# Optimization experiments

Measured on AMD Instinct MI355X. Metric: run time of the kernel, lower is better.

## Reference

```python
import jax, jax.numpy as jnp
import numpy as np

D_MODEL = 1024
NUM_HEADS = 16
HEAD_DIM = D_MODEL // NUM_HEADS


def setup_inputs() -> dict:
    key = jax.random.key(0)
    k_x, k_qw, k_qb, k_ow, k_ob = jax.random.split(key, 5)
    s = 1.0 / np.sqrt(D_MODEL)
    return {
        "x": jax.random.normal(k_x, (2, 2048, D_MODEL), dtype=jnp.float32),
        "qkv_w": jax.random.uniform(k_qw, (3 * D_MODEL, D_MODEL), jnp.float32, -s, s),
        "qkv_b": jax.random.uniform(k_qb, (3 * D_MODEL,), jnp.float32, -s, s),
        "out_w": jax.random.uniform(k_ow, (D_MODEL, D_MODEL), jnp.float32, -s, s),
        "out_b": jax.random.uniform(k_ob, (D_MODEL,), jnp.float32, -s, s),
    }


def reference(x, qkv_w, qkv_b, out_w, out_b):
    B, S, D = x.shape
    # fused QKV projection: [B,S,3D]
    qkv = jnp.einsum("bsd,ed->bse", x, qkv_w) + qkv_b
    # [B,S,H,3*hd] -> [B,H,S,3*hd]
    qkv = qkv.reshape(B, S, NUM_HEADS, 3 * HEAD_DIM).transpose(0, 2, 1, 3)
    q, k, v = jnp.split(qkv, 3, axis=-1)
    scale = 1.0 / jnp.sqrt(jnp.asarray(HEAD_DIM, x.dtype))
    scores = jnp.einsum("bhqd,bhkd->bhqk", q, k) * scale
    attn = jax.nn.softmax(scores, axis=-1)
    vals = jnp.einsum("bhqk,bhkd->bhqd", attn, v)
    vals = vals.transpose(0, 2, 1, 3).reshape(B, S, D)
    return jnp.einsum("bsd,ed->bse", vals, out_w) + out_b
```

## Files before the change

### kernel.cpp

```cpp
#include <hip/hip_runtime.h>
#include <stdint.h>


#define D_MODEL 1024
#define NUM_HEADS 16
#define HEAD_DIM 64
#define BATCH 2
#define SEQ 2048
#define M_TOT (BATCH * SEQ)
#define QKV_N (3 * D_MODEL)

typedef __attribute__((ext_vector_type(8))) short bf16x8;
typedef __attribute__((ext_vector_type(4))) short bf16x4;
typedef __attribute__((ext_vector_type(4))) float f32x4;
typedef __attribute__((ext_vector_type(4))) unsigned int u32x4;

__device__ __forceinline__ unsigned short f2bf(float f) {
    union { float f; unsigned int u; } v; v.f = f;
    unsigned int u = v.u;
    u += 0x7fffu + ((u >> 16) & 1u);
    return (unsigned short)(u >> 16);
}

__device__ __forceinline__ unsigned int exp2_bf16u(float x) {
    return (unsigned int)__builtin_fmaf(x, 128.0f, 16251.58f);
}

__device__ __forceinline__ unsigned int perm_pack(unsigned int hi, unsigned int lo) {
#if __has_builtin(__builtin_amdgcn_perm)
    return __builtin_amdgcn_perm(hi, lo, 0x05040100u);
#else
    return (lo & 0xFFFFu) | (hi << 16);
#endif
}

__device__ __forceinline__ void gld_lds16(const unsigned short* g,
                                          unsigned short* l) {
#if __has_builtin(__builtin_amdgcn_global_load_lds)
    __builtin_amdgcn_global_load_lds(
        (const __attribute__((address_space(1))) unsigned int*)g,
        (__attribute__((address_space(3))) unsigned int*)l, 16, 0, 0);
#else
    *(u32x4*)(l + (threadIdx.x & 63) * 8) = *(const u32x4*)g;
#endif
}

__global__ __launch_bounds__(256) void cvt_all(const float* __restrict__ x,
                                               const float* __restrict__ qw,
                                               const float* __restrict__ ow,
                                               unsigned short* __restrict__ xb,
                                               unsigned short* __restrict__ wqb,
                                               unsigned short* __restrict__ wob) {
    int i = blockIdx.x * 256 + threadIdx.x;
    const int N1 = M_TOT * D_MODEL / 8;
    const int N2 = N1 + QKV_N * D_MODEL / 8;
    const float* src; unsigned short* dst; int j;
    if (i < N1)      { src = x;  dst = xb;  j = i; }
    else if (i < N2) { src = qw; dst = wqb; j = i - N1; }
    else             { src = ow; dst = wob; j = i - N2; }
    const float4* s = (const float4*)src;
    float4 a = s[2 * j], b = s[2 * j + 1];
    u32x4 o;
    o.x = (unsigned int)f2bf(a.x) | ((unsigned int)f2bf(a.y) << 16);
    o.y = (unsigned int)f2bf(a.z) | ((unsigned int)f2bf(a.w) << 16);
    o.z = (unsigned int)f2bf(b.x) | ((unsigned int)f2bf(b.y) << 16);
    o.w = (unsigned int)f2bf(b.z) | ((unsigned int)f2bf(b.w) << 16);
    *(u32x4*)(dst + 8 * (size_t)j) = o;
}

__device__ __forceinline__ void gemm_tile(const unsigned short* __restrict__ A,
                                          const unsigned short* __restrict__ Bw,
                                          int K, int m0, int n0,
                                          unsigned short (*As)[128 * 64],
                                          unsigned short (*Bs)[128 * 64],
                                          f32x4 acc[4][4]) {
    const int tid = threadIdx.x;
    const int lane = tid & 63;
    const int wave = tid >> 6;
    const int wm = (wave >> 1) * 64;
    const int wn = (wave & 1) * 64;
    const int quad = lane >> 4;
    const int l16 = lane & 15;
    const int lrow = lane >> 3;
    const int sw = (lane & 7) ^ (lrow & 7);
    const int l7 = l16 & 7;

#pragma unroll
    for (int mt = 0; mt < 4; mt++)
#pragma unroll
        for (int nt = 0; nt < 4; nt++) acc[mt][nt] = (f32x4)0.0f;

    auto stage = [&](int kt, int b) {
#pragma unroll
        for (int i = 0; i < 4; ++i) {
            int R = wave * 32 + i * 8;
            int grow = R + lrow;
            gld_lds16(A + (size_t)(m0 + grow) * K + kt + sw * 8, As[b] + R * 64);
            gld_lds16(Bw + (size_t)(n0 + grow) * K + kt + sw * 8, Bs[b] + R * 64);
        }
    };

    stage(0, 0);
    __syncthreads();

    const int NT = K / 64;
    for (int t = 0; t < NT; ++t) {
        const int cur = t & 1;
        if (t + 1 < NT) stage((t + 1) * 64, cur ^ 1);
#pragma unroll
        for (int ks = 0; ks < 2; ++ks) {
            int cxl = ((ks * 4 + quad) ^ l7) * 8;
            bf16x8 af[4], bf[4];
#pragma unroll
            for (int mt = 0; mt < 4; mt++)
                af[mt] = *(const bf16x8*)(As[cur] + (wm + mt * 16 + l16) * 64 + cxl);
#pragma unroll
            for (int nt = 0; nt < 4; nt++)
                bf[nt] = *(const bf16x8*)(Bs[cur] + (wn + nt * 16 + l16) * 64 + cxl);
#pragma unroll
            for (int mt = 0; mt < 4; mt++)
#pragma unroll
                for (int nt = 0; nt < 4; nt++)
                    acc[mt][nt] = __builtin_amdgcn_mfma_f32_16x16x32_bf16(
                        af[mt], bf[nt], acc[mt][nt], 0, 0, 0);
        }
        __syncthreads();
    }
}

__global__ __launch_bounds__(256) void gemm_qkv(const unsigned short* __restrict__ xb,
                                                const unsigned short* __restrict__ wb,
                                                const float* __restrict__ bias,
                                                unsigned short* __restrict__ qb,
                                                unsigned short* __restrict__ kb,
                                                unsigned short* __restrict__ vtb) {
    __shared__ __align__(16) unsigned short As[2][128 * 64];
    __shared__ __align__(16) unsigned short Bs[2][128 * 64];
    f32x4 acc[4][4];
    const int m0 = blockIdx.y * 128, n0 = blockIdx.x * 128;
    gemm_tile(xb, wb, D_MODEL, m0, n0, As, Bs, acc);

    const int tid = threadIdx.x;
    const int lane = tid & 63, wave = tid >> 6;
    const int wm = (wave >> 1) * 64, wn = (wave & 1) * 64;
    const int quad = lane >> 4, l16 = lane & 15;
    const float QSCALE = 0.18033688011112042f;

    const int s64 = (n0 + wn) >> 6;
    const int h = s64 / 3;
    const int sec = s64 - h * 3;
    const int bh = (m0 >> 11) * NUM_HEADS + h;
    const int sbase = (m0 + wm) & 2047;

    unsigned short* sm = ((wave & 2) ? Bs[0] : As[0]) + (wave & 1) * 4096;

    if (sec < 2) {
        const float scl = (sec == 0) ? QSCALE : 1.0f;
#pragma unroll
        for (int nt = 0; nt < 4; nt++) {
            int c = nt * 16 + l16;
            float bia = bias[n0 + wn + c];
#pragma unroll
            for (int mt = 0; mt < 4; mt++)
#pragma unroll
                for (int r = 0; r < 4; r++) {
                    int row = mt * 16 + quad * 4 + r;
                    sm[row * 64 + ((((c >> 3) ^ (row & 7)) << 3) | (c & 7))] =
                        f2bf((acc[mt][nt][r] + bia) * scl);
                }
        }
        unsigned short* dstb = (sec == 0) ? qb : kb;
#pragma unroll
        for (int p = 0; p < 8; p++) {
            int row = p * 8 + (lane >> 3);
            int g = lane & 7;
            u32x4 ch = *(const u32x4*)(sm + row * 64 + ((g ^ (row & 7)) << 3));
            *(u32x4*)(dstb + ((size_t)bh * SEQ + sbase + row) * 64 + g * 8) = ch;
        }
    } else {
#pragma unroll
        for (int nt = 0; nt < 4; nt++) {
            int d = nt * 16 + l16;
            float bia = bias[n0 + wn + d];
#pragma unroll
            for (int mt = 0; mt < 4; mt++) {
                int c = mt * 16 + quad * 4;
                unsigned short t4[4];
#pragma unroll
                for (int r = 0; r < 4; r++) t4[r] = f2bf(acc[mt][nt][r] + bia);
                *(uint64_t*)(sm + d * 64 +
                             ((((c >> 3) ^ (d & 7)) << 3) | (c & 7))) =
                    *(const uint64_t*)t4;
            }
        }
#pragma unroll
        for (int p = 0; p < 8; p++) {
            int row = p * 8 + (lane >> 3);
            int g = lane & 7;
            u32x4 ch = *(const u32x4*)(sm + row * 64 + ((g ^ (row & 7)) << 3));
            *(u32x4*)(vtb + ((size_t)bh * 64 + row) * SEQ + sbase + g * 8) = ch;
        }
    }
}

__global__ __launch_bounds__(256) void attn(const unsigned short* __restrict__ qb,
                                            const unsigned short* __restrict__ kb,
                                            const unsigned short* __restrict__ vtb,
                                            unsigned short* __restrict__ vals) {
    __shared__ __align__(16) unsigned short Ks[2][2][64 * 64];
    __shared__ __align__(16) unsigned short VTs[2][2][64 * 64];

    const int tid = threadIdx.x;
    const int lane = tid & 63, wave = tid >> 6;
    const int quad = lane >> 4, l16 = lane & 15;
    const int l7 = l16 & 7;
    const int bh = blockIdx.x;
    const int q0 = blockIdx.y * 128;
    const unsigned short* qh = qb + (size_t)bh * SEQ * 64;
    const unsigned short* kh = kb + (size_t)bh * SEQ * 64;
    const unsigned short* vth = vtb + (size_t)bh * 64 * SEQ;
    const int wrow = wave * 32;

    bf16x8 aq[2][2];
#pragma unroll
    for (int nq = 0; nq < 2; nq++)
#pragma unroll
        for (int ks = 0; ks < 2; ++ks)
            aq[nq][ks] = *(const bf16x8*)(
                qh + (size_t)(q0 + wrow + nq * 16 + l16) * 64 + ks * 32 + quad * 8);

    const int lrow = lane >> 3;
    const int sw = (lane & 7) ^ (lrow & 7);

    int cxl0 = ((0 * 4 + quad) ^ l7) * 8;
    int cxl1 = ((1 * 4 + quad) ^ l7) * 8;

    auto stage = [&](int t, int b) {
        int kt = t * 128;
#pragma unroll
        for (int h = 0; h < 2; ++h) {
            int kth = kt + h * 64;
#pragma unroll
            for (int i = 0; i < 2; ++i) {
                int R = wave * 16 + i * 8;
                int row = R + lrow;
                int krow = (row & 0x23) | ((row & 0x0C) << 1) | ((row & 0x10) >> 2);
                gld_lds16(kh + (size_t)(kth + krow) * 64 + sw * 8,
                          &Ks[b][h][R * 64]);
                gld_lds16(vth + (size_t)row * SEQ + kth + sw * 8,
                          &VTs[b][h][R * 64]);
            }
        }
    };

    stage(0, 0);
    __syncthreads();

    f32x4 oacc[2][4];
    f32x4 lsum[2];
#pragma unroll
    for (int mt = 0; mt < 2; mt++) {
        lsum[mt] = (f32x4)0.0f;
#pragma unroll
        for (int nt = 0; nt < 4; nt++) oacc[mt][nt] = (f32x4)0.0f;
    }

    bf16x8 ones8;
#pragma unroll
    for (int j = 0; j < 8; j++) ones8[j] = (short)0x3F80;

    const int NR = SEQ / 128;
    for (int t = 0; t < NR; ++t) {
        const int cur = t & 1;
        if (t + 1 < NR) stage(t + 1, cur ^ 1);

#pragma unroll
        for (int hf = 0; hf < 2; ++hf) {
            const unsigned short* Kc = Ks[cur][hf];
            const unsigned short* Vc = VTs[cur][hf];

            f32x4 sacc[4][2];
#pragma unroll
            for (int mk = 0; mk < 4; mk++)
#pragma unroll
                for (int nq = 0; nq < 2; nq++) sacc[mk][nq] = (f32x4)0.0f;
#pragma unroll
            for (int ks = 0; ks < 2; ++ks) {
                int cxl = ks ? cxl1 : cxl0;
                bf16x8 bk[4];
#pragma unroll
                for (int mk = 0; mk < 4; mk++)
                    bk[mk] = *(const bf16x8*)(Kc + (mk * 16 + l16) * 64 + cxl);
#pragma unroll
                for (int mk = 0; mk < 4; mk++)
#pragma unroll
                    for (int nq = 0; nq < 2; nq++)
                        sacc[mk][nq] = __builtin_amdgcn_mfma_f32_16x16x32_bf16(
                            bk[mk], aq[nq][ks], sacc[mk][nq], 0, 0, 0);
            }

            bf16x4 pf[4][2];
#pragma unroll
            for (int mk = 0; mk < 4; mk++)
#pragma unroll
                for (int nq = 0; nq < 2; nq++) {
                    unsigned int u0 = exp2_bf16u(sacc[mk][nq][0]);
                    unsigned int u1 = exp2_bf16u(sacc[mk][nq][1]);
                    unsigned int u2 = exp2_bf16u(sacc[mk][nq][2]);
                    unsigned int u3 = exp2_bf16u(sacc[mk][nq][3]);
                    union { unsigned int u[2]; bf16x4 b; } cv;
                    cv.u[0] = perm_pack(u1, u0);
                    cv.u[1] = perm_pack(u3, u2);
                    pf[mk][nq] = cv.b;
                }

#pragma unroll
            for (int w = 0; w < 2; ++w) {
                bf16x8 ap0 = __builtin_shufflevector(
                    pf[2 * w][0], pf[2 * w + 1][0], 0, 1, 2, 3, 4, 5, 6, 7);
                bf16x8 ap1 = __builtin_shufflevector(
                    pf[2 * w][1], pf[2 * w + 1][1], 0, 1, 2, 3, 4, 5, 6, 7);
                int cxl = w ? cxl1 : cxl0;
#pragma unroll
                for (int nt = 0; nt < 4; nt++) {
                    bf16x8 bv = *(const bf16x8*)(Vc + (nt * 16 + l16) * 64 + cxl);
                    oacc[0][nt] = __builtin_amdgcn_mfma_f32_16x16x32_bf16(
                        ap0, bv, oacc[0][nt], 0, 0, 0);
                    oacc[1][nt] = __builtin_amdgcn_mfma_f32_16x16x32_bf16(
                        ap1, bv, oacc[1][nt], 0, 0, 0);
                }
                lsum[0] = __builtin_amdgcn_mfma_f32_16x16x32_bf16(
                    ap0, ones8, lsum[0], 0, 0, 0);
                lsum[1] = __builtin_amdgcn_mfma_f32_16x16x32_bf16(
                    ap1, ones8, lsum[1], 0, 0, 0);
            }
        }
        __syncthreads();
    }

    const int b = bh >> 4, h = bh & 15;
#pragma unroll
    for (int mt = 0; mt < 2; mt++) {
        f32x4 inv;
#pragma unroll
        for (int r = 0; r < 4; r++) inv[r] = 1.0f / lsum[mt][r];
#pragma unroll
        for (int nt = 0; nt < 4; nt++) {
            int d = nt * 16 + l16;
#pragma unroll
            for (int r = 0; r < 4; r++) {
                int row = wrow + mt * 16 + quad * 4 + r;
                float v = oacc[mt][nt][r] * inv[r];
                vals[((size_t)(b * SEQ + q0 + row)) * D_MODEL + h * 64 + d] =
                    f2bf(v);
            }
        }
    }
}

__global__ __launch_bounds__(256) void gemm_out(const unsigned short* __restrict__ vb,
                                                const unsigned short* __restrict__ wb,
                                                const float* __restrict__ bias,
                                                float* __restrict__ out) {
    __shared__ __align__(16) unsigned short As[2][128 * 64];
    __shared__ __align__(16) unsigned short Bs[2][64 * 64];
    const int tid = threadIdx.x;
    const int lane = tid & 63, wave = tid >> 6;
    const int wm = (wave >> 1) * 64, wn = (wave & 1) * 32;
    const int quad = lane >> 4, l16 = lane & 15;
    const int lrow = lane >> 3;
    const int sw = (lane & 7) ^ (lrow & 7);
    const int l7 = l16 & 7;
    const int m0 = blockIdx.y * 128, n0 = blockIdx.x * 64;

    f32x4 acc[4][2];
#pragma unroll
    for (int mt = 0; mt < 4; mt++)
#pragma unroll
        for (int nt = 0; nt < 2; nt++) acc[mt][nt] = (f32x4)0.0f;

    auto stage = [&](int kt, int b) {
#pragma unroll
        for (int i = 0; i < 4; ++i) {
            int R = wave * 32 + i * 8;
            gld_lds16(vb + (size_t)(m0 + R + lrow) * D_MODEL + kt + sw * 8,
                      As[b] + R * 64);
        }
#pragma unroll
        for (int i = 0; i < 2; ++i) {
            int R = wave * 16 + i * 8;
            gld_lds16(wb + (size_t)(n0 + R + lrow) * D_MODEL + kt + sw * 8,
                      Bs[b] + R * 64);
        }
    };

    stage(0, 0);
    __syncthreads();

    const int NT = D_MODEL / 64;
    for (int t = 0; t < NT; ++t) {
        const int cur = t & 1;
        if (t + 1 < NT) stage((t + 1) * 64, cur ^ 1);
#pragma unroll
        for (int ks = 0; ks < 2; ++ks) {
            int cxl = ((ks * 4 + quad) ^ l7) * 8;
            bf16x8 af[4], bf[2];
#pragma unroll
            for (int mt = 0; mt < 4; mt++)
                af[mt] = *(const bf16x8*)(As[cur] + (wm + mt * 16 + l16) * 64 + cxl);
#pragma unroll
            for (int nt = 0; nt < 2; nt++)
                bf[nt] = *(const bf16x8*)(Bs[cur] + (wn + nt * 16 + l16) * 64 + cxl);
#pragma unroll
            for (int mt = 0; mt < 4; mt++)
#pragma unroll
                for (int nt = 0; nt < 2; nt++)
                    acc[mt][nt] = __builtin_amdgcn_mfma_f32_16x16x32_bf16(
                        af[mt], bf[nt], acc[mt][nt], 0, 0, 0);
        }
        __syncthreads();
    }

#pragma unroll
    for (int mt = 0; mt < 4; mt++)
#pragma unroll
        for (int nt = 0; nt < 2; nt++) {
            int n = n0 + wn + nt * 16 + l16;
            float bia = bias[n];
#pragma unroll
            for (int r = 0; r < 4; r++) {
                int m = m0 + wm + mt * 16 + quad * 4 + r;
                out[(size_t)m * D_MODEL + n] = acc[mt][nt][r] + bia;
            }
        }
}

extern "C" void kernel_launch(void* const* d_in, const int* in_sizes, int n_in,
                              void* d_out, int out_size, void* d_ws, size_t ws_size,
                              hipStream_t stream) {
    const float* x = (const float*)d_in[0];
    const float* qkv_w = (const float*)d_in[1];
    const float* qkv_b = (const float*)d_in[2];
    const float* out_w = (const float*)d_in[3];
    const float* out_b = (const float*)d_in[4];
    float* out = (float*)d_out;

    char* ws = (char*)d_ws;
    size_t off = 0;
    auto carve = [&](size_t bytes) -> void* {
        void* p = ws + off;
        off += (bytes + 255) & ~(size_t)255;
        return p;
    };
    unsigned short* xb  = (unsigned short*)carve((size_t)M_TOT * D_MODEL * 2);
    unsigned short* wqb = (unsigned short*)carve((size_t)QKV_N * D_MODEL * 2);
    unsigned short* wob = (unsigned short*)carve((size_t)D_MODEL * D_MODEL * 2);
    unsigned short* qbuf = (unsigned short*)carve((size_t)M_TOT * D_MODEL * 2);
    unsigned short* kbuf = (unsigned short*)carve((size_t)M_TOT * D_MODEL * 2);
    unsigned short* vtb  = (unsigned short*)carve((size_t)M_TOT * D_MODEL * 2);
    unsigned short* vals = xb;

    const int NCHUNK = (M_TOT + QKV_N + D_MODEL) * D_MODEL / 8;
    cvt_all<<<NCHUNK / 256, 256, 0, stream>>>(x, qkv_w, out_w, xb, wqb, wob);

    gemm_qkv<<<dim3(QKV_N / 128, M_TOT / 128), 256, 0, stream>>>(
        xb, wqb, qkv_b, qbuf, kbuf, vtb);

    attn<<<dim3(BATCH * NUM_HEADS, SEQ / 128), 256, 0, stream>>>(
        qbuf, kbuf, vtb, vals);

    gemm_out<<<dim3(D_MODEL / 64, M_TOT / 128), 256, 0, stream>>>(
        vals, wob, out_b, out);
}
```

Baseline: 184.6 us.

## Retile QKV GEMM to 256x192 per-head blocks with finer-grained pipelined loads

The QKV projection GEMM now uses 512-thread blocks computing 256x192 tiles, so each block covers one full head (Q, K and V slices). This replaces the 128x128 tiles with 256 threads. The K loop splits staging into quarter-steps with explicit vmcnt waits and raw barriers, and raises wave priority around the MFMA bursts so loads overlap compute. The epilogue writes Q, K and transposed V for the whole head through shared memory in one pass. The aim is better operand reuse and less barrier stall, at the cost of more registers per thread, larger LDS use, and reliance on hand-counted waitcnt values.

Result: faster. 171.4 us (-7.2%).

```diff
diff --git a/kernel.cpp b/kernel.cpp
--- a/kernel.cpp
+++ b/kernel.cpp
@@ -68,138 +68,150 @@
     *(u32x4*)(dst + 8 * (size_t)j) = o;
 }
 
-__device__ __forceinline__ void gemm_tile(const unsigned short* __restrict__ A,
-                                          const unsigned short* __restrict__ Bw,
-                                          int K, int m0, int n0,
-                                          unsigned short (*As)[128 * 64],
-                                          unsigned short (*Bs)[128 * 64],
-                                          f32x4 acc[4][4]) {
-    const int tid = threadIdx.x;
-    const int lane = tid & 63;
-    const int wave = tid >> 6;
-    const int wm = (wave >> 1) * 64;
-    const int wn = (wave & 1) * 64;
-    const int quad = lane >> 4;
-    const int l16 = lane & 15;
-    const int lrow = lane >> 3;
-    const int sw = (lane & 7) ^ (lrow & 7);
-    const int l7 = l16 & 7;
-
-#pragma unroll
-    for (int mt = 0; mt < 4; mt++)
-#pragma unroll
-        for (int nt = 0; nt < 4; nt++) acc[mt][nt] = (f32x4)0.0f;
-
-    auto stage = [&](int kt, int b) {
-#pragma unroll
-        for (int i = 0; i < 4; ++i) {
-            int R = wave * 32 + i * 8;
-            int grow = R + lrow;
-            gld_lds16(A + (size_t)(m0 + grow) * K + kt + sw * 8, As[b] + R * 64);
-            gld_lds16(Bw + (size_t)(n0 + grow) * K + kt + sw * 8, Bs[b] + R * 64);
-        }
-    };
-
-    stage(0, 0);
-    __syncthreads();
-
-    const int NT = K / 64;
-    for (int t = 0; t < NT; ++t) {
-        const int cur = t & 1;
-        if (t + 1 < NT) stage((t + 1) * 64, cur ^ 1);
-#pragma unroll
-        for (int ks = 0; ks < 2; ++ks) {
-            int cxl = ((ks * 4 + quad) ^ l7) * 8;
-            bf16x8 af[4], bf[4];
-#pragma unroll
-            for (int mt = 0; mt < 4; mt++)
-                af[mt] = *(const bf16x8*)(As[cur] + (wm + mt * 16 + l16) * 64 + cxl);
-#pragma unroll
-            for (int nt = 0; nt < 4; nt++)
-                bf[nt] = *(const bf16x8*)(Bs[cur] + (wn + nt * 16 + l16) * 64 + cxl);
-#pragma unroll
-            for (int mt = 0; mt < 4; mt++)
-#pragma unroll
-                for (int nt = 0; nt < 4; nt++)
-                    acc[mt][nt] = __builtin_amdgcn_mfma_f32_16x16x32_bf16(
-                        af[mt], bf[nt], acc[mt][nt], 0, 0, 0);
-        }
-        __syncthreads();
-    }
-}
-
-__global__ __launch_bounds__(256) void gemm_qkv(const unsigned short* __restrict__ xb,
-                                                const unsigned short* __restrict__ wb,
-                                                const float* __restrict__ bias,
-                                                unsigned short* __restrict__ qb,
-                                                unsigned short* __restrict__ kb,
-                                                unsigned short* __restrict__ vtb) {
-    __shared__ __align__(16) unsigned short As[2][128 * 64];
-    __shared__ __align__(16) unsigned short Bs[2][128 * 64];
-    f32x4 acc[4][4];
-    const int m0 = blockIdx.y * 128, n0 = blockIdx.x * 128;
-    gemm_tile(xb, wb, D_MODEL, m0, n0, As, Bs, acc);
+__global__ __launch_bounds__(512, 2) void gemm_qkv(const unsigned short* __restrict__ xb,
+                                                   const unsigned short* __restrict__ wb,
+                                                   const float* __restrict__ bias,
+                                                   unsigned short* __restrict__ qb,
+                                                   unsigned short* __restrict__ kb,
+                                                   unsigned short* __restrict__ vtb) {
+    __shared__ __align__(16) unsigned short L[57344];
 
     const int tid = threadIdx.x;
     const int lane = tid & 63, wave = tid >> 6;
-    const int wm = (wave >> 1) * 64, wn = (wave & 1) * 64;
-    const int quad = lane >> 4, l16 = lane & 15;
+    const int quad = lane >> 4, l16 = lane & 15, l7 = l16 & 7;
+    const int lrow = lane >> 3;
+    const int sw = (lane & 7) ^ lrow;
+    const int m0 = blockIdx.x * 256;
+    const int n0 = blockIdx.y * 192;
+    const int wmr = (wave >> 2) * 128;
+    const int wn = (wave & 3) * 48;
+
+    float biasr[3];
+#pragma unroll
+    for (int nt = 0; nt < 3; nt++) biasr[nt] = bias[n0 + wn + nt * 16 + l16];
+
+    f32x4 acc[8][3];
+#pragma unroll
+    for (int m = 0; m < 8; m++)
+#pragma unroll
+        for (int nt = 0; nt < 3; nt++) acc[m][nt] = (f32x4)0.0f;
+
+    auto stA = [&](int tt, int s, int b) {
+        int R = s * 64 + wave * 8 + lrow;
+        gld_lds16(xb + (size_t)(m0 + R) * D_MODEL + tt * 64 + sw * 8,
+                  L + b * 16384 + (s * 64 + wave * 8) * 64);
+    };
+    auto stB = [&](int tt, int s, int b) {
+        int R = s * 64 + wave * 8 + lrow;
+        gld_lds16(wb + (size_t)(n0 + R) * D_MODEL + tt * 64 + sw * 8,
+                  L + 32768 + b * 12288 + (s * 64 + wave * 8) * 64);
+    };
+
+    stB(0, 0, 0); stB(0, 1, 0); stB(0, 2, 0);
+    stA(0, 0, 0); stA(0, 1, 0); stA(0, 2, 0); stA(0, 3, 0);
+
+    const int NT = D_MODEL / 64;
+    for (int t = 0; t < NT; ++t) {
+        const int cb = t & 1, nb = cb ^ 1;
+        const int tn = (t + 1 < NT) ? t + 1 : NT - 1;
+        const unsigned short* Ac = L + cb * 16384;
+        const unsigned short* Bc = L + 32768 + cb * 12288;
+        bf16x8 bfr[3][2];
+
+#pragma unroll
+        for (int q = 0; q < 4; ++q) {
+            if (q == 0) {
+                asm volatile("s_waitcnt vmcnt(1)" ::: "memory");
+                asm volatile("s_barrier" ::: "memory");
+            } else if (q == 2) {
+                asm volatile("s_waitcnt vmcnt(4)" ::: "memory");
+                asm volatile("s_barrier" ::: "memory");
+            }
+            if (q == 0)      { stB(tn, 0, nb); stB(tn, 1, nb); }
+            else if (q == 1) { stB(tn, 2, nb); stA(tn, 0, nb); }
+            else if (q == 2) { stA(tn, 1, nb); stA(tn, 2, nb); }
+            else             { stA(tn, 3, nb); }
+
+            if (q == 0) {
+#pragma unroll
+                for (int nt = 0; nt < 3; nt++)
+#pragma unroll
+                    for (int ks = 0; ks < 2; ++ks)
+                        bfr[nt][ks] = *(const bf16x8*)(
+                            Bc + (wn + nt * 16 + l16) * 64 + ((ks * 4 + quad) ^ l7) * 8);
+            }
+            bf16x8 afr[2][2];
+#pragma unroll
+            for (int j = 0; j < 2; ++j)
+#pragma unroll
+                for (int ks = 0; ks < 2; ++ks)
+                    afr[j][ks] = *(const bf16x8*)(
+                        Ac + (wmr + (q * 2 + j) * 16 + l16) * 64 + ((ks * 4 + quad) ^ l7) * 8);
+
+            __builtin_amdgcn_s_setprio(1);
+#pragma unroll
+            for (int j = 0; j < 2; ++j)
+#pragma unroll
+                for (int nt = 0; nt < 3; nt++)
+#pragma unroll
+                    for (int ks = 0; ks < 2; ++ks)
+                        acc[q * 2 + j][nt] = __builtin_amdgcn_mfma_f32_16x16x32_bf16(
+                            afr[j][ks], bfr[nt][ks], acc[q * 2 + j][nt], 0, 0, 0);
+            __builtin_amdgcn_s_setprio(0);
+        }
+    }
+
+    __syncthreads();
+
     const float QSCALE = 0.18033688011112042f;
-
-    const int s64 = (n0 + wn) >> 6;
-    const int h = s64 / 3;
-    const int sec = s64 - h * 3;
-    const int bh = (m0 >> 11) * NUM_HEADS + h;
-    const int sbase = (m0 + wm) & 2047;
-
-    unsigned short* sm = ((wave & 2) ? Bs[0] : As[0]) + (wave & 1) * 4096;
-
-    if (sec < 2) {
-        const float scl = (sec == 0) ? QSCALE : 1.0f;
-#pragma unroll
-        for (int nt = 0; nt < 4; nt++) {
-            int c = nt * 16 + l16;
-            float bia = bias[n0 + wn + c];
-#pragma unroll
-            for (int mt = 0; mt < 4; mt++)
+#pragma unroll
+    for (int nt = 0; nt < 3; nt++) {
+        int colb = wn + nt * 16;
+        int sec = colb >> 6;
+        int c64 = (colb & 63) + l16;
+        float bia = biasr[nt];
+        if (sec < 2) {
+            unsigned short* img = L + sec * 16384;
+            float scl = sec ? 1.0f : QSCALE;
+#pragma unroll
+            for (int mt = 0; mt < 8; mt++)
 #pragma unroll
                 for (int r = 0; r < 4; r++) {
-                    int row = mt * 16 + quad * 4 + r;
-                    sm[row * 64 + ((((c >> 3) ^ (row & 7)) << 3) | (c & 7))] =
+                    int row = wmr + mt * 16 + quad * 4 + r;
+                    img[row * 64 + ((((c64 >> 3) ^ (row & 7)) << 3) | (c64 & 7))] =
                         f2bf((acc[mt][nt][r] + bia) * scl);
                 }
-        }
-        unsigned short* dstb = (sec == 0) ? qb : kb;
-#pragma unroll
-        for (int p = 0; p < 8; p++) {
-            int row = p * 8 + (lane >> 3);
-            int g = lane & 7;
-            u32x4 ch = *(const u32x4*)(sm + row * 64 + ((g ^ (row & 7)) << 3));
-            *(u32x4*)(dstb + ((size_t)bh * SEQ + sbase + row) * 64 + g * 8) = ch;
-        }
-    } else {
-#pragma unroll
-        for (int nt = 0; nt < 4; nt++) {
-            int d = nt * 16 + l16;
-            float bia = bias[n0 + wn + d];
-#pragma unroll
-            for (int mt = 0; mt < 4; mt++) {
-                int c = mt * 16 + quad * 4;
+        } else {
+            unsigned short* img = L + 32768;
+            int d = c64;
+#pragma unroll
+            for (int mt = 0; mt < 8; mt++) {
+                int cs = wmr + mt * 16 + quad * 4;
+                int sb = cs >> 6, c64s = cs & 63;
                 unsigned short t4[4];
 #pragma unroll
                 for (int r = 0; r < 4; r++) t4[r] = f2bf(acc[mt][nt][r] + bia);
-                *(uint64_t*)(sm + d * 64 +
-                             ((((c >> 3) ^ (d & 7)) << 3) | (c & 7))) =
+                *(uint64_t*)(img + (d * 4 + sb) * 64 +
+                             ((((c64s >> 3) ^ (d & 7)) << 3) | (c64s & 7))) =
                     *(const uint64_t*)t4;
             }
         }
-#pragma unroll
-        for (int p = 0; p < 8; p++) {
-            int row = p * 8 + (lane >> 3);
-            int g = lane & 7;
-            u32x4 ch = *(const u32x4*)(sm + row * 64 + ((g ^ (row & 7)) << 3));
-            *(u32x4*)(vtb + ((size_t)bh * 64 + row) * SEQ + sbase + g * 8) = ch;
-        }
+    }
+    __syncthreads();
+
+    const int bh = (m0 >> 11) * NUM_HEADS + blockIdx.y;
+    const int sbase = m0 & 2047;
+    const int g = lane & 7;
+#pragma unroll
+    for (int p = 0; p < 4; p++) {
+        int rr = p * 64 + wave * 8 + (lane >> 3);
+        u32x4 ch = *(const u32x4*)(L + rr * 64 + ((g ^ (rr & 7)) << 3));
+        *(u32x4*)(qb + ((size_t)bh * SEQ + sbase + rr) * 64 + g * 8) = ch;
+        ch = *(const u32x4*)(L + 16384 + rr * 64 + ((g ^ (rr & 7)) << 3));
+        *(u32x4*)(kb + ((size_t)bh * SEQ + sbase + rr) * 64 + g * 8) = ch;
+        int d = rr >> 2, sb = rr & 3;
+        ch = *(const u32x4*)(L + 32768 + rr * 64 + ((g ^ (d & 7)) << 3));
+        *(u32x4*)(vtb + ((size_t)bh * 64 + d) * SEQ + sbase + sb * 64 + g * 8) = ch;
     }
 }
 
@@ -463,7 +475,7 @@
     const int NCHUNK = (M_TOT + QKV_N + D_MODEL) * D_MODEL / 8;
     cvt_all<<<NCHUNK / 256, 256, 0, stream>>>(x, qkv_w, out_w, xb, wqb, wob);
 
-    gemm_qkv<<<dim3(QKV_N / 128, M_TOT / 128), 256, 0, stream>>>(
+    gemm_qkv<<<dim3(M_TOT / 256, QKV_N / 192), 512, 0, stream>>>(
         xb, wqb, qkv_b, qbuf, kbuf, vtb);
 
     attn<<<dim3(BATCH * NUM_HEADS, SEQ / 128), 256, 0, stream>>>(
```
